# Performance work log

Hardware: AMD Instinct MI355X
Metric: run time of the kernel (lower is better)

## Reference

```python
import jax, jax.numpy as jnp
import numpy as np

B, S, D_IN, D_OUT = 4, 4096, 256, 64


def setup_inputs() -> dict:
    key = jax.random.key(0)
    k1, k2, k3, k4, k5, k6 = jax.random.split(key, 6)
    return {
        "inputs_for_keys": jax.random.normal(k1, (B, S, D_IN), dtype=jnp.float32),
        "inputs_for_values": jax.random.normal(k2, (B, S, D_IN), dtype=jnp.float32),
        "inputs_for_queries": jax.random.normal(k3, (B, S, D_IN), dtype=jnp.float32),
        "wq": jax.random.normal(k4, (D_IN, D_OUT), dtype=jnp.float32) * 0.05,
        "wk": jax.random.normal(k5, (D_IN, D_OUT), dtype=jnp.float32) * 0.05,
        "wv": jax.random.normal(k6, (D_IN, D_OUT), dtype=jnp.float32) * 0.05,
    }


def reference(inputs_for_keys, inputs_for_values, inputs_for_queries, wq, wk, wv):
    # Linear projections: [B,S,D_IN] x [D_IN,D_OUT] -> [B,S,D_OUT]
    K = jnp.einsum("bsd,de->bse", inputs_for_keys, wk)
    V = jnp.einsum("bsd,de->bse", inputs_for_values, wv)
    Q = jnp.einsum("bsd,de->bse", inputs_for_queries, wq)
    d = K.shape[2]
    # Scaled dot-product scores: [B, S_q, S_k]
    scores = jnp.einsum("bqe,bke->bqk", Q, K) / jnp.sqrt(jnp.float32(d))
    # Causal mask: -inf where key index j > query index i (strict upper triangle)
    q_idx = jnp.arange(Q.shape[1])[:, None]
    k_idx = jnp.arange(K.shape[1])[None, :]
    mask = jnp.where(k_idx > q_idx, -jnp.inf, 0.0).astype(scores.dtype)
    scores = scores + mask[None, :, :]
    weights = jax.nn.softmax(scores, axis=-1)
    return jnp.einsum("bqk,bke->bqe", weights, V)
```

## Files before the change

### kernel.cpp

```cpp
#include <hip/hip_runtime.h>

#define S_LEN 4096
#define D_IN 256
#define D_OUT 64
#define BATCH 4
#define BQ 128
#define NQT (S_LEN / BQ)

typedef short bf16x8 __attribute__((ext_vector_type(8)));
typedef float f32x4 __attribute__((ext_vector_type(4)));

union L16 { int4 i; bf16x8 s; ushort u[8]; };
union U8  { uint2 d; ushort u[4]; };

#define SWZ(row, chunk) (((row) << 7) + ((((chunk) ^ ((row) & 7))) << 4))

#define QSCALE 0.1803368801111137f

__device__ inline ushort f2bf(float x) {
    unsigned u = __builtin_bit_cast(unsigned, x);
    u += 0x7FFFu + ((u >> 16) & 1u);
    return (ushort)(u >> 16);
}
__device__ inline ushort f2bf_t(float x) {
    return (ushort)(__builtin_bit_cast(unsigned, x) >> 16);
}
__device__ inline float bf2f(ushort h) {
    return __builtin_bit_cast(float, (unsigned)h << 16);
}

__global__ __launch_bounds__(256) void wsplit_kernel(
    const float* __restrict__ wq, const float* __restrict__ wk, const float* __restrict__ wv,
    ushort* __restrict__ Wt)
{
    const float* W = (blockIdx.y == 0) ? wq : (blockIdx.y == 1) ? wk : wv;
    __shared__ float Ws[64][68];
    const int t  = threadIdx.x;
    const int k0 = blockIdx.x * 64;
#pragma unroll
    for (int i = 0; i < 4; ++i) {
        int idx = t + i * 256;
        int r = idx >> 4, c4 = (idx & 15) * 4;
        *reinterpret_cast<float4*>(&Ws[r][c4]) =
            *reinterpret_cast<const float4*>(&W[(size_t)(k0 + r) * 64 + c4]);
    }
    __syncthreads();
    const int n = t >> 2, kc = t & 3;
    ushort h[16];
#pragma unroll
    for (int i = 0; i < 16; ++i) h[i] = f2bf(Ws[kc * 16 + i][n]);
    ushort* dst = Wt + ((size_t)blockIdx.y * 64 + n) * 256 + k0 + kc * 16;
    *reinterpret_cast<int4*>(dst)     = *reinterpret_cast<int4*>(h);
    *reinterpret_cast<int4*>(dst + 8) = *reinterpret_cast<int4*>(h + 8);
}

__global__ __launch_bounds__(256) void proj_kernel(
    const float* __restrict__ Xq, const float* __restrict__ Xk, const float* __restrict__ Xv,
    const ushort* __restrict__ Wt,
    ushort* __restrict__ Qb, ushort* __restrict__ Kb, ushort* __restrict__ Vtb)
{
    const float* X = (blockIdx.y == 0) ? Xq : (blockIdx.y == 1) ? Xk : Xv;
    const ushort* Wtp = Wt + (size_t)blockIdx.y * 64 * 256;

    __shared__ __align__(16) ushort Ob[64][64];

    const int t    = threadIdx.x;
    const int lane = t & 63;
    const int w    = t >> 6;
    const int n    = lane & 15;
    const int g    = lane >> 4;
    const int row0 = blockIdx.x * 64;

    const float* xrow = X + (size_t)(row0 + 16 * w + n) * D_IN;

    f32x4 acc[4];
    const f32x4 zero4 = {0.f, 0.f, 0.f, 0.f};
#pragma unroll
    for (int nt = 0; nt < 4; ++nt) acc[nt] = zero4;

#pragma unroll
    for (int kt = 0; kt < 8; ++kt) {
        const float4 c0 = *reinterpret_cast<const float4*>(xrow + kt * 32 + 8 * g);
        const float4 c1 = *reinterpret_cast<const float4*>(xrow + kt * 32 + 8 * g + 4);
        L16 wb[4];
#pragma unroll
        for (int nt = 0; nt < 4; ++nt)
            wb[nt].i = *reinterpret_cast<const int4*>(
                &Wtp[(size_t)(16 * nt + n) * 256 + kt * 32 + 8 * g]);

        const float xv[8] = {c0.x, c0.y, c0.z, c0.w, c1.x, c1.y, c1.z, c1.w};
        L16 xh, xl;
#pragma unroll
        for (int i = 0; i < 8; ++i) {
            ushort h = f2bf(xv[i]);
            xh.u[i] = h;
            xl.u[i] = f2bf(xv[i] - bf2f(h));
        }
#pragma unroll
        for (int nt = 0; nt < 4; ++nt) {
            acc[nt] = __builtin_amdgcn_mfma_f32_16x16x32_bf16(xh.s, wb[nt].s, acc[nt], 0, 0, 0);
            acc[nt] = __builtin_amdgcn_mfma_f32_16x16x32_bf16(xl.s, wb[nt].s, acc[nt], 0, 0, 0);
        }
    }

    const bool isV = (blockIdx.y == 2);
    const float oscale = (blockIdx.y == 0) ? QSCALE : 1.0f;
#pragma unroll
    for (int j = 0; j < 4; ++j) {
#pragma unroll
        for (int nt = 0; nt < 4; ++nt) {
            ushort h = f2bf(acc[nt][j] * oscale);
            int r = 16 * w + 4 * g + j;
            int c = 16 * nt + n;
            if (isV) Ob[c][r] = h; else Ob[r][c] = h;
        }
    }
    __syncthreads();
    const int b  = row0 >> 12;
    const int s0 = row0 & 4095;
#pragma unroll
    for (int i = 0; i < 2; ++i) {
        int idx = t + i * 256;
        int r = idx >> 3, c8 = (idx & 7) * 8;
        int4 v = *reinterpret_cast<const int4*>(&Ob[r][c8]);
        if (blockIdx.y == 0)
            *reinterpret_cast<int4*>(&Qb[(size_t)(row0 + r) * 64 + c8]) = v;
        else if (blockIdx.y == 1)
            *reinterpret_cast<int4*>(&Kb[(size_t)(row0 + r) * 64 + c8]) = v;
        else
            *reinterpret_cast<int4*>(&Vtb[((size_t)b * 64 + r) * S_LEN + s0 + c8]) = v;
    }
}

__global__ __launch_bounds__(256) void attn_kernel(
    const ushort* __restrict__ Q, const ushort* __restrict__ K,
    const ushort* __restrict__ Vt, float* __restrict__ O,
    ushort* __restrict__ Opart, float* __restrict__ Mpart, float* __restrict__ Lpart,
    int chunk_keys, int NCH, int lr4q, int Llive)
{
    __shared__ __align__(16) ushort Ks[64 * 64];
    __shared__ __align__(16) ushort Vs[64 * 64];
    __shared__ __align__(16) ushort Ps[4 * 32 * 64];

    const int Rq = 1 << lr4q;

    const int b = blockIdx.x & 3;
    const int f = blockIdx.x >> 2;
    int c = 0;
    while (NQT * (c + 1) - ((Rq * (c + 1) * c) >> 1) <= f) ++c;
    const int off  = NQT * c - ((Rq * c * (c - 1)) >> 1);
    const int qt   = (NQT - 1) - (f - off);
    const int ch   = c;
    const int q0   = qt * BQ;
    const int c0   = ch * chunk_keys;
    const int nchq = (qt >> lr4q) + 1;

    const int t    = threadIdx.x;
    const int lane = t & 63;
    const int w    = t >> 6;
    const int n    = lane & 15;
    const int g    = lane >> 4;

    const int kend = (c0 + chunk_keys < q0 + BQ) ? c0 + chunk_keys : q0 + BQ;
    const int kt0  = c0 >> 6;
    const int kt1  = (kend + 63) >> 6;

    const ushort* Qp = Q  + (size_t)b * S_LEN * 64;
    const ushort* Kp = K  + (size_t)b * S_LEN * 64;
    const ushort* Vp = Vt + (size_t)b * 64 * S_LEN;

    char* KsB = (char*)Ks;
    char* VsB = (char*)Vs;
    char* PsB = (char*)Ps + w * 4096;

    const int wqmin = q0 + 32 * w;
    const int wqmax = wqmin + 31;

    L16 aq[2][2];
#pragma unroll
    for (int h = 0; h < 2; ++h) {
        const size_t qr = (size_t)(wqmin + 16 * h + n) * 64;
        aq[h][0].i = *reinterpret_cast<const int4*>(&Qp[qr + 8 * g]);
        aq[h][1].i = *reinterpret_cast<const int4*>(&Qp[qr + 32 + 8 * g]);
    }

    f32x4 oacc[2][4];
    const f32x4 zero4 = {0.f, 0.f, 0.f, 0.f};
#pragma unroll
    for (int h = 0; h < 2; ++h)
#pragma unroll
        for (int nt = 0; nt < 4; ++nt) oacc[h][nt] = zero4;
    float mreg[2] = {-1e30f, -1e30f}, lreg[2] = {0.f, 0.f};

    const int srow = t >> 3, sc = t & 7;

    int4 kv[2], vv[2];
    {
        const int k0 = kt0 << 6;
#pragma unroll
        for (int i = 0; i < 2; ++i) {
            int row = srow + i * 32;
            kv[i] = *reinterpret_cast<const int4*>(&Kp[(size_t)(k0 + row) * 64 + sc * 8]);
            vv[i] = *reinterpret_cast<const int4*>(&Vp[(size_t)row * S_LEN + k0 + sc * 8]);
        }
    }

    for (int kt = kt0; kt < kt1; ++kt) {
        const int k0 = kt << 6;
        __syncthreads();
#pragma unroll
        for (int i = 0; i < 2; ++i) {
            int row = srow + i * 32;
            *reinterpret_cast<int4*>(KsB + SWZ(row, sc)) = kv[i];
            *reinterpret_cast<int4*>(VsB + SWZ(row, sc)) = vv[i];
        }
        if (kt + 1 < kt1) {
            const int k0n = (kt + 1) << 6;
#pragma unroll
            for (int i = 0; i < 2; ++i) {
                int row = srow + i * 32;
                kv[i] = *reinterpret_cast<const int4*>(&Kp[(size_t)(k0n + row) * 64 + sc * 8]);
                vv[i] = *reinterpret_cast<const int4*>(&Vp[(size_t)row * S_LEN + k0n + sc * 8]);
            }
        }
        __syncthreads();
        if (k0 > wqmax) continue;

        f32x4 cS[2][4];
#pragma unroll
        for (int t4 = 0; t4 < 4; ++t4) {
            L16 k0f, k1f;
            k0f.i = *reinterpret_cast<const int4*>(KsB + SWZ(16 * t4 + n, g));
            k1f.i = *reinterpret_cast<const int4*>(KsB + SWZ(16 * t4 + n, 4 + g));
#pragma unroll
            for (int h = 0; h < 2; ++h) {
                f32x4 z = zero4;
                z          = __builtin_amdgcn_mfma_f32_16x16x32_bf16(k0f.s, aq[h][0].s, z, 0, 0, 0);
                cS[h][t4]  = __builtin_amdgcn_mfma_f32_16x16x32_bf16(k1f.s, aq[h][1].s, z, 0, 0, 0);
            }
        }

#pragma unroll
        for (int h = 0; h < 2; ++h) {
            const int qrow = wqmin + 16 * h + n;
            float sc4[4][4];
#pragma unroll
            for (int t4 = 0; t4 < 4; ++t4)
#pragma unroll
                for (int j = 0; j < 4; ++j) sc4[t4][j] = cS[h][t4][j];
            if (k0 + 63 > qrow) {
                const int kb = k0 + 4 * g;
#pragma unroll
                for (int t4 = 0; t4 < 4; ++t4)
#pragma unroll
                    for (int j = 0; j < 4; ++j)
                        if (kb + 16 * t4 + j > qrow) sc4[t4][j] = -1e30f;
            }

            float m0 = fmaxf(fmaxf(sc4[0][0], sc4[0][1]), fmaxf(sc4[0][2], sc4[0][3]));
            float m1 = fmaxf(fmaxf(sc4[1][0], sc4[1][1]), fmaxf(sc4[1][2], sc4[1][3]));
            float m2 = fmaxf(fmaxf(sc4[2][0], sc4[2][1]), fmaxf(sc4[2][2], sc4[2][3]));
            float m3 = fmaxf(fmaxf(sc4[3][0], sc4[3][1]), fmaxf(sc4[3][2], sc4[3][3]));
            float mx = fmaxf(fmaxf(m0, m1), fmaxf(m2, m3));
            mx = fmaxf(mx, __shfl_xor(mx, 16, 64));
            mx = fmaxf(mx, __shfl_xor(mx, 32, 64));

            if (__any(mx > mreg[h] + 8.f)) {
                const float mnew  = fmaxf(mreg[h], mx);
                const float alpha = exp2f(mreg[h] - mnew);
                mreg[h] = mnew;
                lreg[h] *= alpha;
#pragma unroll
                for (int nt = 0; nt < 4; ++nt)
#pragma unroll
                    for (int j = 0; j < 4; ++j) oacc[h][nt][j] *= alpha;
            }

            float psum = 0.f;
#pragma unroll
            for (int t4 = 0; t4 < 4; ++t4) {
                U8 pw;
#pragma unroll
                for (int j = 0; j < 4; ++j) {
                    const float p = exp2f(sc4[t4][j] - mreg[h]);
                    pw.u[j] = f2bf_t(p);
                    psum   += p;
                }
                *reinterpret_cast<uint2*>(PsB + SWZ(16 * h + n, 2 * t4 + (g >> 1)) + 8 * (g & 1)) = pw.d;
            }
            psum += __shfl_xor(psum, 16, 64);
            psum += __shfl_xor(psum, 32, 64);
            lreg[h] += psum;
        }

        asm volatile("s_waitcnt lgkmcnt(0)" ::: "memory");
        L16 pa[2][2];
#pragma unroll
        for (int h = 0; h < 2; ++h) {
            pa[h][0].i = *reinterpret_cast<const int4*>(PsB + SWZ(16 * h + n, g));
            pa[h][1].i = *reinterpret_cast<const int4*>(PsB + SWZ(16 * h + n, 4 + g));
        }
#pragma unroll
        for (int nt = 0; nt < 4; ++nt) {
            L16 bv0, bv1;
            bv0.i = *reinterpret_cast<const int4*>(VsB + SWZ(16 * nt + n, g));
            bv1.i = *reinterpret_cast<const int4*>(VsB + SWZ(16 * nt + n, 4 + g));
#pragma unroll
            for (int h = 0; h < 2; ++h) {
                oacc[h][nt] = __builtin_amdgcn_mfma_f32_16x16x32_bf16(bv0.s, pa[h][0].s, oacc[h][nt], 0, 0, 0);
                oacc[h][nt] = __builtin_amdgcn_mfma_f32_16x16x32_bf16(bv1.s, pa[h][1].s, oacc[h][nt], 0, 0, 0);
            }
        }
    }

    if (nchq == 1) {
#pragma unroll
        for (int h = 0; h < 2; ++h) {
            const float inv = 1.f / lreg[h];
            float* orow = O + ((size_t)b * S_LEN + wqmin + 16 * h + n) * 64;
#pragma unroll
            for (int nt = 0; nt < 4; ++nt)
#pragma unroll
                for (int j = 0; j < 4; ++j)
                    orow[16 * nt + 4 * g + j] = oacc[h][nt][j] * inv;
        }
    } else {
        const size_t slot = (size_t)((qt << 2) | b) * NCH + ch;
#pragma unroll
        for (int h = 0; h < 2; ++h)
#pragma unroll
            for (int nt = 0; nt < 4; ++nt) {
                U8 pw;
#pragma unroll
                for (int j = 0; j < 4; ++j) pw.u[j] = f2bf(oacc[h][nt][j]);
                *reinterpret_cast<uint2*>(PsB + SWZ(16 * h + n, 2 * nt + (g >> 1)) + 8 * (g & 1)) = pw.d;
            }
        asm volatile("s_waitcnt lgkmcnt(0)" ::: "memory");
        ushort* dst = Opart + slot * (BQ * 64) + w * 2048;
#pragma unroll
        for (int i = 0; i < 4; ++i) {
            int ii = i * 64 + lane;
            *reinterpret_cast<int4*>(dst + ii * 8) =
                *reinterpret_cast<const int4*>((const char*)PsB + ii * 16);
        }
        if (g == 0) {
#pragma unroll
            for (int h = 0; h < 2; ++h) {
                Mpart[slot * BQ + 32 * w + 16 * h + n] = mreg[h];
                Lpart[slot * BQ + 32 * w + 16 * h + n] = lreg[h];
            }
        }
    }
}

__global__ __launch_bounds__(256) void reduce_kernel(
    const ushort* __restrict__ Opart, const float* __restrict__ Mpart,
    const float* __restrict__ Lpart, float* __restrict__ O,
    int NCH, int chunk_keys)
{
    const int bx  = blockIdx.x >> 2;
    const int seg = blockIdx.x & 3;
    const int b   = bx & 3;
    const int qt  = bx >> 2;
    const int q0  = qt * BQ;
    const int nch = (q0 + BQ + chunk_keys - 1) / chunk_keys;
    if (nch <= 1) return;

    const int t    = threadIdx.x;
    const int row  = seg * 32 + (t >> 3);
    const int c8   = t & 7;
    const int wv   = row >> 5, rl = row & 31;
    const int cswz = (c8 ^ (rl & 7)) << 4;

    const size_t mbase = (size_t)bx * NCH * BQ + row;
    float mmax = -1e30f;
    for (int ch = 0; ch < nch; ++ch)
        mmax = fmaxf(mmax, Mpart[mbase + (size_t)ch * BQ]);

    float ltot = 0.f;
    float acc[8];
#pragma unroll
    for (int i = 0; i < 8; ++i) acc[i] = 0.f;

    for (int ch = 0; ch < nch; ++ch) {
        const float wgt = exp2f(Mpart[mbase + (size_t)ch * BQ] - mmax);
        ltot += wgt * Lpart[mbase + (size_t)ch * BQ];
        const char* ob = (const char*)(Opart + ((size_t)bx * NCH + ch) * (BQ * 64))
                         + wv * 4096 + rl * 128 + cswz;
        L16 v;
        v.i = *reinterpret_cast<const int4*>(ob);
#pragma unroll
        for (int i = 0; i < 8; ++i) acc[i] += wgt * bf2f(v.u[i]);
    }
    const float inv = 1.f / ltot;
    float* dst = O + ((size_t)b * S_LEN + q0 + row) * 64 + c8 * 8;
#pragma unroll
    for (int i = 0; i < 2; ++i) {
        float4 o = make_float4(acc[4 * i] * inv, acc[4 * i + 1] * inv,
                               acc[4 * i + 2] * inv, acc[4 * i + 3] * inv);
        *reinterpret_cast<float4*>(dst + i * 4) = o;
    }
}

extern "C" void kernel_launch(void* const* d_in, const int* in_sizes, int n_in,
                              void* d_out, int out_size, void* d_ws, size_t ws_size,
                              hipStream_t stream) {
    const float* Xk = (const float*)d_in[0];
    const float* Xv = (const float*)d_in[1];
    const float* Xq = (const float*)d_in[2];
    const float* wq = (const float*)d_in[3];
    const float* wk = (const float*)d_in[4];
    const float* wv = (const float*)d_in[5];
    float* out = (float*)d_out;

    const size_t NEL = (size_t)BATCH * S_LEN * D_OUT;
    ushort* Qb  = (ushort*)d_ws;
    ushort* Kb  = Qb + NEL;
    ushort* Vtb = Kb + NEL;
    const size_t base_bytes = 3 * NEL * sizeof(ushort);
    const size_t per_nch    = (size_t)BATCH * NQT *
                              (BQ * 64 * sizeof(ushort) + 2 * BQ * sizeof(float));

    int NCH = 1;
    if      (ws_size >= base_bytes + 16 * per_nch) NCH = 16;
    else if (ws_size >= base_bytes +  8 * per_nch) NCH = 8;
    else if (ws_size >= base_bytes +  4 * per_nch) NCH = 4;
    else if (ws_size >= base_bytes +  2 * per_nch) NCH = 2;
    const int chunk_keys = S_LEN / NCH;
    const int Rq = chunk_keys / BQ;
    int lr4q = 0; while ((1 << lr4q) < Rq) ++lr4q;
    const int Llive = NCH * NQT - Rq * ((NCH * (NCH - 1)) >> 1);

    ushort* Wt    = (ushort*)((char*)d_ws + base_bytes);
    ushort* Opart = (ushort*)((char*)d_ws + base_bytes);
    float*  Mpart = (float*)((char*)d_ws + base_bytes +
                             (size_t)BATCH * NQT * NCH * BQ * 64 * sizeof(ushort));
    float*  Lpart = Mpart + (size_t)BATCH * NQT * NCH * BQ;

    wsplit_kernel<<<dim3(4, 3), 256, 0, stream>>>(wq, wk, wv, Wt);

    proj_kernel<<<dim3(BATCH * S_LEN / 64, 3), 256, 0, stream>>>(
        Xq, Xk, Xv, Wt, Qb, Kb, Vtb);

    attn_kernel<<<4 * Llive, 256, 0, stream>>>(Qb, Kb, Vtb, out, Opart, Mpart, Lpart,
                                               chunk_keys, NCH, lr4q, Llive);
    if (NCH > 1)
        reduce_kernel<<<BATCH * NQT * 4, 256, 0, stream>>>(Opart, Mpart, Lpart, out,
                                                           NCH, chunk_keys);
}
```

Before: 82.76 us.

## Double-buffer K/V tiles in LDS with one barrier per iteration

Doubles the K and V shared-memory tiles so the next tile is stored to the alternate buffer while the current one is consumed, cutting the per-iteration barriers from two to one. The P staging buffer shrinks to 16 rows per wave, and the PV MFMA is issued per half right after its softmax. s_setprio hints are added around the MFMA blocks. LDS use stays about the same, but the per-half P round trip adds waitcnt serialisation and fewer MFMAs are in flight per V fragment load.

```diff
diff --git a/kernel.cpp b/kernel.cpp
--- a/kernel.cpp
+++ b/kernel.cpp
@@ -138,9 +138,9 @@
     ushort* __restrict__ Opart, float* __restrict__ Mpart, float* __restrict__ Lpart,
     int chunk_keys, int NCH, int lr4q, int Llive)
 {
-    __shared__ __align__(16) ushort Ks[64 * 64];
-    __shared__ __align__(16) ushort Vs[64 * 64];
-    __shared__ __align__(16) ushort Ps[4 * 32 * 64];
+    __shared__ __align__(16) ushort Ks[2][64 * 64];
+    __shared__ __align__(16) ushort Vs[2][64 * 64];
+    __shared__ __align__(16) ushort Ps[4 * 16 * 64];
 
     const int Rq = 1 << lr4q;
 
@@ -169,9 +169,7 @@
     const ushort* Kp = K  + (size_t)b * S_LEN * 64;
     const ushort* Vp = Vt + (size_t)b * 64 * S_LEN;
 
-    char* KsB = (char*)Ks;
-    char* VsB = (char*)Vs;
-    char* PsB = (char*)Ps + w * 4096;
+    char* PsB = (char*)Ps + w * 2048;
 
     const int wqmin = q0 + 32 * w;
     const int wqmax = wqmin + 31;
@@ -194,123 +192,130 @@
 
     const int srow = t >> 3, sc = t & 7;
 
-    int4 kv[2], vv[2];
-    {
-        const int k0 = kt0 << 6;
+    auto load_tile = [&](int4 (&kr)[2], int4 (&vr)[2], int kt_) {
+        const int kk0 = kt_ << 6;
 #pragma unroll
         for (int i = 0; i < 2; ++i) {
             int row = srow + i * 32;
-            kv[i] = *reinterpret_cast<const int4*>(&Kp[(size_t)(k0 + row) * 64 + sc * 8]);
-            vv[i] = *reinterpret_cast<const int4*>(&Vp[(size_t)row * S_LEN + k0 + sc * 8]);
-        }
-    }
-
+            kr[i] = *reinterpret_cast<const int4*>(&Kp[(size_t)(kk0 + row) * 64 + sc * 8]);
+            vr[i] = *reinterpret_cast<const int4*>(&Vp[(size_t)row * S_LEN + kk0 + sc * 8]);
+        }
+    };
+    auto store_tile = [&](int buf, const int4 (&kr)[2], const int4 (&vr)[2]) {
+        char* kb = (char*)Ks + buf * 8192;
+        char* vb = (char*)Vs + buf * 8192;
+#pragma unroll
+        for (int i = 0; i < 2; ++i) {
+            int row = srow + i * 32;
+            *reinterpret_cast<int4*>(kb + SWZ(row, sc)) = kr[i];
+            *reinterpret_cast<int4*>(vb + SWZ(row, sc)) = vr[i];
+        }
+    };
+
+    int4 kv[2], vv[2];
+    load_tile(kv, vv, kt0);
+    store_tile(0, kv, vv);
+    if (kt0 + 1 < kt1) load_tile(kv, vv, kt0 + 1);
+    __syncthreads();
+
+    int cur = 0;
     for (int kt = kt0; kt < kt1; ++kt) {
         const int k0 = kt << 6;
+        if (kt + 1 < kt1) {
+            store_tile(cur ^ 1, kv, vv);
+            if (kt + 2 < kt1) load_tile(kv, vv, kt + 2);
+        }
+
+        if (k0 <= wqmax) {
+            char* KsB = (char*)Ks + cur * 8192;
+            char* VsB = (char*)Vs + cur * 8192;
+
+            f32x4 cS[2][4];
+            __builtin_amdgcn_s_setprio(1);
+#pragma unroll
+            for (int t4 = 0; t4 < 4; ++t4) {
+                L16 k0f, k1f;
+                k0f.i = *reinterpret_cast<const int4*>(KsB + SWZ(16 * t4 + n, g));
+                k1f.i = *reinterpret_cast<const int4*>(KsB + SWZ(16 * t4 + n, 4 + g));
+#pragma unroll
+                for (int h = 0; h < 2; ++h) {
+                    f32x4 z = zero4;
+                    z          = __builtin_amdgcn_mfma_f32_16x16x32_bf16(k0f.s, aq[h][0].s, z, 0, 0, 0);
+                    cS[h][t4]  = __builtin_amdgcn_mfma_f32_16x16x32_bf16(k1f.s, aq[h][1].s, z, 0, 0, 0);
+                }
+            }
+            __builtin_amdgcn_s_setprio(0);
+
+#pragma unroll
+            for (int h = 0; h < 2; ++h) {
+                const int qrow = wqmin + 16 * h + n;
+                float sc4[4][4];
+#pragma unroll
+                for (int t4 = 0; t4 < 4; ++t4)
+#pragma unroll
+                    for (int j = 0; j < 4; ++j) sc4[t4][j] = cS[h][t4][j];
+                if (k0 + 63 > qrow) {
+                    const int kb = k0 + 4 * g;
+#pragma unroll
+                    for (int t4 = 0; t4 < 4; ++t4)
+#pragma unroll
+                        for (int j = 0; j < 4; ++j)
+                            if (kb + 16 * t4 + j > qrow) sc4[t4][j] = -1e30f;
+                }
+
+                float m0 = fmaxf(fmaxf(sc4[0][0], sc4[0][1]), fmaxf(sc4[0][2], sc4[0][3]));
+                float m1 = fmaxf(fmaxf(sc4[1][0], sc4[1][1]), fmaxf(sc4[1][2], sc4[1][3]));
+                float m2 = fmaxf(fmaxf(sc4[2][0], sc4[2][1]), fmaxf(sc4[2][2], sc4[2][3]));
+                float m3 = fmaxf(fmaxf(sc4[3][0], sc4[3][1]), fmaxf(sc4[3][2], sc4[3][3]));
+                float mx = fmaxf(fmaxf(m0, m1), fmaxf(m2, m3));
+                mx = fmaxf(mx, __shfl_xor(mx, 16, 64));
+                mx = fmaxf(mx, __shfl_xor(mx, 32, 64));
+
+                if (__any(mx > mreg[h] + 8.f)) {
+                    const float mnew  = fmaxf(mreg[h], mx);
+                    const float alpha = exp2f(mreg[h] - mnew);
+                    mreg[h] = mnew;
+                    lreg[h] *= alpha;
+#pragma unroll
+                    for (int nt = 0; nt < 4; ++nt)
+#pragma unroll
+                        for (int j = 0; j < 4; ++j) oacc[h][nt][j] *= alpha;
+                }
+
+                float psum = 0.f;
+#pragma unroll
+                for (int t4 = 0; t4 < 4; ++t4) {
+                    U8 pw;
+#pragma unroll
+                    for (int j = 0; j < 4; ++j) {
+                        const float p = exp2f(sc4[t4][j] - mreg[h]);
+                        pw.u[j] = f2bf_t(p);
+                        psum   += p;
+                    }
+                    *reinterpret_cast<uint2*>(PsB + SWZ(n, 2 * t4 + (g >> 1)) + 8 * (g & 1)) = pw.d;
+                }
+                psum += __shfl_xor(psum, 16, 64);
+                psum += __shfl_xor(psum, 32, 64);
+                lreg[h] += psum;
+
+                asm volatile("s_waitcnt lgkmcnt(0)" ::: "memory");
+                L16 pa0, pa1;
+                pa0.i = *reinterpret_cast<const int4*>(PsB + SWZ(n, g));
+                pa1.i = *reinterpret_cast<const int4*>(PsB + SWZ(n, 4 + g));
+                __builtin_amdgcn_s_setprio(1);
+#pragma unroll
+                for (int nt = 0; nt < 4; ++nt) {
+                    L16 bv0, bv1;
+                    bv0.i = *reinterpret_cast<const int4*>(VsB + SWZ(16 * nt + n, g));
+                    bv1.i = *reinterpret_cast<const int4*>(VsB + SWZ(16 * nt + n, 4 + g));
+                    oacc[h][nt] = __builtin_amdgcn_mfma_f32_16x16x32_bf16(bv0.s, pa0.s, oacc[h][nt], 0, 0, 0);
+                    oacc[h][nt] = __builtin_amdgcn_mfma_f32_16x16x32_bf16(bv1.s, pa1.s, oacc[h][nt], 0, 0, 0);
+                }
+                __builtin_amdgcn_s_setprio(0);
+            }
+        }
         __syncthreads();
-#pragma unroll
-        for (int i = 0; i < 2; ++i) {
-            int row = srow + i * 32;
-            *reinterpret_cast<int4*>(KsB + SWZ(row, sc)) = kv[i];
-            *reinterpret_cast<int4*>(VsB + SWZ(row, sc)) = vv[i];
-        }
-        if (kt + 1 < kt1) {
-            const int k0n = (kt + 1) << 6;
-#pragma unroll
-            for (int i = 0; i < 2; ++i) {
-                int row = srow + i * 32;
-                kv[i] = *reinterpret_cast<const int4*>(&Kp[(size_t)(k0n + row) * 64 + sc * 8]);
-                vv[i] = *reinterpret_cast<const int4*>(&Vp[(size_t)row * S_LEN + k0n + sc * 8]);
-            }
-        }
-        __syncthreads();
-        if (k0 > wqmax) continue;
-
-        f32x4 cS[2][4];
-#pragma unroll
-        for (int t4 = 0; t4 < 4; ++t4) {
-            L16 k0f, k1f;
-            k0f.i = *reinterpret_cast<const int4*>(KsB + SWZ(16 * t4 + n, g));
-            k1f.i = *reinterpret_cast<const int4*>(KsB + SWZ(16 * t4 + n, 4 + g));
-#pragma unroll
-            for (int h = 0; h < 2; ++h) {
-                f32x4 z = zero4;
-                z          = __builtin_amdgcn_mfma_f32_16x16x32_bf16(k0f.s, aq[h][0].s, z, 0, 0, 0);
-                cS[h][t4]  = __builtin_amdgcn_mfma_f32_16x16x32_bf16(k1f.s, aq[h][1].s, z, 0, 0, 0);
-            }
-        }
-
-#pragma unroll
-        for (int h = 0; h < 2; ++h) {
-            const int qrow = wqmin + 16 * h + n;
-            float sc4[4][4];
-#pragma unroll
-            for (int t4 = 0; t4 < 4; ++t4)
-#pragma unroll
-                for (int j = 0; j < 4; ++j) sc4[t4][j] = cS[h][t4][j];
-            if (k0 + 63 > qrow) {
-                const int kb = k0 + 4 * g;
-#pragma unroll
-                for (int t4 = 0; t4 < 4; ++t4)
-#pragma unroll
-                    for (int j = 0; j < 4; ++j)
-                        if (kb + 16 * t4 + j > qrow) sc4[t4][j] = -1e30f;
-            }
-
-            float m0 = fmaxf(fmaxf(sc4[0][0], sc4[0][1]), fmaxf(sc4[0][2], sc4[0][3]));
-            float m1 = fmaxf(fmaxf(sc4[1][0], sc4[1][1]), fmaxf(sc4[1][2], sc4[1][3]));
-            float m2 = fmaxf(fmaxf(sc4[2][0], sc4[2][1]), fmaxf(sc4[2][2], sc4[2][3]));
-            float m3 = fmaxf(fmaxf(sc4[3][0], sc4[3][1]), fmaxf(sc4[3][2], sc4[3][3]));
-            float mx = fmaxf(fmaxf(m0, m1), fmaxf(m2, m3));
-            mx = fmaxf(mx, __shfl_xor(mx, 16, 64));
-            mx = fmaxf(mx, __shfl_xor(mx, 32, 64));
-
-            if (__any(mx > mreg[h] + 8.f)) {
-                const float mnew  = fmaxf(mreg[h], mx);
-                const float alpha = exp2f(mreg[h] - mnew);
-                mreg[h] = mnew;
-                lreg[h] *= alpha;
-#pragma unroll
-                for (int nt = 0; nt < 4; ++nt)
-#pragma unroll
-                    for (int j = 0; j < 4; ++j) oacc[h][nt][j] *= alpha;
-            }
-
-            float psum = 0.f;
-#pragma unroll
-            for (int t4 = 0; t4 < 4; ++t4) {
-                U8 pw;
-#pragma unroll
-                for (int j = 0; j < 4; ++j) {
-                    const float p = exp2f(sc4[t4][j] - mreg[h]);
-                    pw.u[j] = f2bf_t(p);
-                    psum   += p;
-                }
-                *reinterpret_cast<uint2*>(PsB + SWZ(16 * h + n, 2 * t4 + (g >> 1)) + 8 * (g & 1)) = pw.d;
-            }
-            psum += __shfl_xor(psum, 16, 64);
-            psum += __shfl_xor(psum, 32, 64);
-            lreg[h] += psum;
-        }
-
-        asm volatile("s_waitcnt lgkmcnt(0)" ::: "memory");
-        L16 pa[2][2];
-#pragma unroll
-        for (int h = 0; h < 2; ++h) {
-            pa[h][0].i = *reinterpret_cast<const int4*>(PsB + SWZ(16 * h + n, g));
-            pa[h][1].i = *reinterpret_cast<const int4*>(PsB + SWZ(16 * h + n, 4 + g));
-        }
-#pragma unroll
-        for (int nt = 0; nt < 4; ++nt) {
-            L16 bv0, bv1;
-            bv0.i = *reinterpret_cast<const int4*>(VsB + SWZ(16 * nt + n, g));
-            bv1.i = *reinterpret_cast<const int4*>(VsB + SWZ(16 * nt + n, 4 + g));
-#pragma unroll
-            for (int h = 0; h < 2; ++h) {
-                oacc[h][nt] = __builtin_amdgcn_mfma_f32_16x16x32_bf16(bv0.s, pa[h][0].s, oacc[h][nt], 0, 0, 0);
-                oacc[h][nt] = __builtin_amdgcn_mfma_f32_16x16x32_bf16(bv1.s, pa[h][1].s, oacc[h][nt], 0, 0, 0);
-            }
-        }
+        cur ^= 1;
     }
 
     if (nchq == 1) {
@@ -327,21 +332,22 @@
     } else {
         const size_t slot = (size_t)((qt << 2) | b) * NCH + ch;
 #pragma unroll
-        for (int h = 0; h < 2; ++h)
+        for (int h = 0; h < 2; ++h) {
 #pragma unroll
             for (int nt = 0; nt < 4; ++nt) {
                 U8 pw;
 #pragma unroll
                 for (int j = 0; j < 4; ++j) pw.u[j] = f2bf(oacc[h][nt][j]);
-                *reinterpret_cast<uint2*>(PsB + SWZ(16 * h + n, 2 * nt + (g >> 1)) + 8 * (g & 1)) = pw.d;
+                *reinterpret_cast<uint2*>(PsB + SWZ(n, 2 * nt + (g >> 1)) + 8 * (g & 1)) = pw.d;
             }
-        asm volatile("s_waitcnt lgkmcnt(0)" ::: "memory");
-        ushort* dst = Opart + slot * (BQ * 64) + w * 2048;
-#pragma unroll
-        for (int i = 0; i < 4; ++i) {
-            int ii = i * 64 + lane;
-            *reinterpret_cast<int4*>(dst + ii * 8) =
-                *reinterpret_cast<const int4*>((const char*)PsB + ii * 16);
+            asm volatile("s_waitcnt lgkmcnt(0)" ::: "memory");
+            ushort* dst = Opart + slot * (BQ * 64) + w * 2048 + h * 1024;
+#pragma unroll
+            for (int i = 0; i < 2; ++i) {
+                int ii = i * 64 + lane;
+                *reinterpret_cast<int4*>(dst + ii * 8) =
+                    *reinterpret_cast<const int4*>((const char*)PsB + ii * 16);
+            }
         }
         if (g == 0) {
 #pragma unroll
```

After: 83.11 us. About the same (+0.4%).
